# Performance work log

Measured on AMD Instinct MI355X. Metric: run time of the kernel, lower is better.

The kernel has to match this reference:

```python
import jax, jax.numpy as jnp
import numpy as np
from jax import lax

K, N, DV, NBPS, NITER, BATCH = 1056, 2112, 5, 4, 20, 1024
M = N - K            # number of parity checks
E = M * (DV + 1)     # Tanner-graph edges (H = [A | I_m], row weight DV+1)
NSYM = N // NBPS     # QAM symbols per codeword


def _qam16():
    # Sionna-style Gray-mapped QAM constellation, unit average energy.
    def pam_gray(b):
        if len(b) > 1:
            return (1 - 2 * b[0]) * (2 ** (len(b) - 1) - pam_gray(b[1:]))
        return 1 - 2 * b[0]
    pts = []
    for i in range(2 ** NBPS):
        b = [(i >> (NBPS - 1 - j)) & 1 for j in range(NBPS)]
        pts.append(complex(pam_gray(b[0::2]), pam_gray(b[1::2])))
    pts = np.asarray(pts)
    pts = pts / np.sqrt(np.mean(np.abs(pts) ** 2))
    return pts.real.astype(np.float32), pts.imag.astype(np.float32)


def setup_inputs() -> dict:
    key = jax.random.key(0)
    rng = np.random.default_rng(0)
    bits = jnp.asarray(rng.integers(0, 2, size=(BATCH, K)), jnp.int32)
    # sparse A: DV distinct info-bit columns per check row
    a_idx = np.argsort(rng.random((M, K)), axis=1)[:, :DV].astype(np.int32)
    edge_vn = np.concatenate([a_idx, K + np.arange(M, dtype=np.int32)[:, None]], axis=1).reshape(-1)
    edge_cn = np.repeat(np.arange(M, dtype=np.int32), DV + 1)
    pre, pim = _qam16()
    k1, k2 = jax.random.split(key)
    return {
        "bits": bits,
        "a_idx": jnp.asarray(a_idx),
        "edge_cn": jnp.asarray(edge_cn),
        "edge_vn": jnp.asarray(edge_vn),
        "points_re": jnp.asarray(pre),
        "points_im": jnp.asarray(pim),
        "noise_re": jax.random.normal(k1, (BATCH, NSYM), jnp.float32),
        "noise_im": jax.random.normal(k2, (BATCH, NSYM), jnp.float32),
        "ebno_db": jnp.float32(4.0),
    }


def _forward(bits, a_idx, edge_cn, edge_vn, points_re, points_im, noise_re, noise_im, ebno_db):
    B = bits.shape[0]
    coderate = K / N
    # ebnodb2no (Es = 1): N0 = 1 / (EbN0_lin * coderate * bits_per_symbol)
    no = 1.0 / (10.0 ** (ebno_db / 10.0) * coderate * NBPS)
    # --- LDPC encode: H = [A | I], parity_i = XOR of info bits in row i ---
    parity = jnp.sum(bits[:, a_idx], axis=-1) % 2          # [B, M]
    cw = jnp.concatenate([bits, parity], axis=1)           # [B, N]
    # --- QAM map ---
    w = jnp.array([1 << (NBPS - 1 - j) for j in range(NBPS)], jnp.int32)
    sym = jnp.sum(cw.reshape(B, NSYM, NBPS) * w, axis=-1)  # [B, S]
    sigma = jnp.sqrt(no / 2.0)
    y_re = points_re[sym] + sigma * noise_re
    y_im = points_im[sym] + sigma * noise_im
    # --- APP demap: LLR = log p(b=0|y) - log p(b=1|y) ---
    d2 = (y_re[..., None] - points_re) ** 2 + (y_im[..., None] - points_im) ** 2  # [B,S,16]
    lg = (-d2 / no)[..., None]                                                     # [B,S,16,1]
    lab = (jnp.arange(2 ** NBPS)[:, None] >> jnp.arange(NBPS - 1, -1, -1)) & 1     # [16,4]
    NEG = jnp.float32(-1e30)
    l0 = jax.nn.logsumexp(jnp.where(lab == 0, lg, NEG), axis=2)
    l1 = jax.nn.logsumexp(jnp.where(lab == 1, lg, NEG), axis=2)
    llr = (l0 - l1).reshape(B, N)                          # [B, N]
    # --- sum-product BP, flooding schedule, NITER iterations ---
    def marg(c2v):  # scatter-add check->variable messages onto variable nodes
        return jnp.zeros((B, N), c2v.dtype).at[:, edge_vn].add(c2v)
    def step(c2v, _):
        v2c = (llr + marg(c2v))[:, edge_vn] - c2v          # extrinsic VN->CN [B,E]
        av = jnp.clip(jnp.abs(v2c), 1e-6, 20.0)
        lt = jnp.log(jnp.tanh(av * 0.5))                   # log|tanh(.)| <= 0
        sg = (v2c < 0).astype(v2c.dtype)
        cs = jnp.zeros((B, M), v2c.dtype).at[:, edge_cn].add(lt)
        ns = jnp.zeros((B, M), v2c.dtype).at[:, edge_cn].add(sg)
        ex = jnp.exp(jnp.minimum(cs[:, edge_cn] - lt, -1e-7))   # prod over other edges < 1
        sp = 1.0 - 2.0 * jnp.mod(ns[:, edge_cn] - sg, 2.0)      # sign product over other edges
        return sp * 2.0 * jnp.arctanh(ex), None
    c2v, _ = lax.scan(step, jnp.zeros((B, E), jnp.float32), None, length=NITER)
    tot = llr + marg(c2v)
    bits_rx = (tot[:, :K] < 0).astype(jnp.float32)         # hard_out=True
    return bits.astype(jnp.float32), bits_rx, tot[:, :K]


def reference(bits, a_idx, edge_cn, edge_vn, points_re, points_im, noise_re, noise_im, ebno_db):
    b, brx, _ = _forward(bits, a_idx, edge_cn, edge_vn, points_re, points_im,
                         noise_re, noise_im, ebno_db)
    return b, brx
```

## Files before the change

kernel.cpp:

```cpp
#include <hip/hip_runtime.h>

#define K_     1056
#define N_     2112
#define M_     1056
#define E_     6336
#define NIE_   5280
#define CAP_   6336
#define ALL_   7392
#define DV_    5
#define ROW_   6
#define NSYM_  528
#define NITER_ 20
#define BATCH_ 1024
#define BS_    512

#define LOG2E_ 1.4426950408889634f
#define AVLO_  (1e-6f * LOG2E_)
#define AVHI_  (20.0f * LOG2E_)
#define QC_    0.99999988f

__device__ __forceinline__ int seg_stride(int d) { return d | 1; }

__device__ __forceinline__ float fexp2(float x) { return __builtin_amdgcn_exp2f(x); }
__device__ __forceinline__ float flog2(float x) { return __builtin_amdgcn_logf(x); }
__device__ __forceinline__ float frcp(float x)  { return __builtin_amdgcn_rcpf(x); }

__global__ __launch_bounds__(BS_, 8) void link_kernel(
    const int*   __restrict__ bits,
    const int*   __restrict__ a_idx,
    const float* __restrict__ points_re,
    const float* __restrict__ points_im,
    const float* __restrict__ noise_re,
    const float* __restrict__ noise_im,
    const float* __restrict__ ebno_db,
    const int*   __restrict__ edge_vn,
    float*       __restrict__ out)
{
#pragma clang fp contract(off)
    const int b   = blockIdx.x;
    const int tid = threadIdx.x;

    __shared__ float s_all[ALL_];
    __shared__ float s_pre[16];
    __shared__ float s_pim[16];
    __shared__ int   s_hist[32];
    __shared__ int   s_binStart[32];
    __shared__ int   s_binBase[32];

    float* s_mem  = s_all;
    float* s_marg = s_all + CAP_;

    int* sc        = (int*)(s_all + N_);
    int* s_deg     = sc;
    int* s_perm    = sc + K_;
    int* s_offslot = sc + 2 * K_;
    int* s_cnt     = sc + 3 * K_;

    if (tid < 16) {
        s_pre[tid] = points_re[tid];
        s_pim[tid] = points_im[tid];
    }
    if (tid < 32) s_hist[tid] = 0;

    const float eb    = ebno_db[0];
    const float no    = 1.0f / ((powf(10.0f, eb / 10.0f) * 0.5f) * 4.0f);
    const float sigma = sqrtf(no / 2.0f);

    for (int i = tid; i < K_; i += BS_) {
        int v = bits[b * K_ + i];
        s_mem[i] = (float)v;
        out[b * K_ + i] = (float)v;
    }
    __syncthreads();

    for (int m = tid; m < M_; m += BS_) {
        float acc = 0.0f;
        #pragma unroll
        for (int d = 0; d < DV_; ++d) acc += s_mem[a_idx[m * DV_ + d]];
        s_mem[K_ + m] = (float)(((int)acc) & 1);
    }
    for (int v = tid; v < K_; v += BS_) { s_deg[v] = 0; s_cnt[v] = 0; }
    __syncthreads();

    for (int s = tid; s < NSYM_; s += BS_) {
        int c0 = (int)s_mem[4 * s + 0];
        int c1 = (int)s_mem[4 * s + 1];
        int c2 = (int)s_mem[4 * s + 2];
        int c3 = (int)s_mem[4 * s + 3];
        int sym = c0 * 8 + c1 * 4 + c2 * 2 + c3;
        float yre = s_pre[sym] + sigma * noise_re[b * NSYM_ + s];
        float yim = s_pim[sym] + sigma * noise_im[b * NSYM_ + s];
        float m0[4], m1[4];
        #pragma unroll
        for (int j = 0; j < 4; ++j) { m0[j] = -1e30f; m1[j] = -1e30f; }
        #pragma unroll
        for (int p = 0; p < 16; ++p) {
            float dre  = yre - s_pre[p];
            float dim_ = yim - s_pim[p];
            float lg   = -(dre * dre + dim_ * dim_) / no;
            #pragma unroll
            for (int j = 0; j < 4; ++j) {
                if (((p >> (3 - j)) & 1) == 0) m0[j] = fmaxf(m0[j], lg);
                else                           m1[j] = fmaxf(m1[j], lg);
            }
        }
        float sum0[4] = {0.0f, 0.0f, 0.0f, 0.0f};
        float sum1[4] = {0.0f, 0.0f, 0.0f, 0.0f};
        #pragma unroll
        for (int p = 0; p < 16; ++p) {
            float dre  = yre - s_pre[p];
            float dim_ = yim - s_pim[p];
            float lg   = -(dre * dre + dim_ * dim_) / no;
            #pragma unroll
            for (int j = 0; j < 4; ++j) {
                if (((p >> (3 - j)) & 1) == 0) sum0[j] += __expf(lg - m0[j]);
                else                           sum1[j] += __expf(lg - m1[j]);
            }
        }
        #pragma unroll
        for (int j = 0; j < 4; ++j) {
            float llr = (m0[j] + __logf(sum0[j])) - (m1[j] + __logf(sum1[j]));
            s_mem[4 * s + j] = llr * LOG2E_;
        }
    }
    for (int idx = tid; idx < NIE_; idx += BS_) {
        int m = idx / 5, j = idx - m * 5;
        atomicAdd(&s_deg[edge_vn[m * ROW_ + j]], 1);
    }
    __syncthreads();

    for (int v = tid; v < K_; v += BS_) atomicAdd(&s_hist[s_deg[v] & 31], 1);
    __syncthreads();
    if (tid == 0) {
        int accS = 0, accB = 0;
        for (int d = 0; d < 32; ++d) {
            int c = s_hist[d];
            s_binStart[d] = accS;
            s_binBase[d]  = accB;
            s_hist[d]     = accS;
            accS += c;
            accB += c * seg_stride(d);
        }
    }
    __syncthreads();
    for (int v = tid; v < K_; v += BS_) {
        int d    = s_deg[v];
        int slot = atomicAdd(&s_hist[d & 31], 1);
        int base = s_binBase[d] + (slot - s_binStart[d]) * seg_stride(d);
        s_perm[slot]  = v | (d << 16);
        s_offslot[v]  = base | (slot << 16);
    }
    __syncthreads();

    int      pv[3];
    unsigned od[3];
    float    lr[3];
    #pragma unroll
    for (int k = 0; k < 3; ++k) {
        int s = tid + BS_ * k;
        if (s < K_) {
            int w = s_perm[s];
            int v = w & 0xFFFF;
            int d = w >> 16;
            int base = s_binBase[d] + (s - s_binStart[d]) * seg_stride(d);
            pv[k] = v;
            od[k] = (unsigned)base | ((unsigned)d << 16);
            lr[k] = s_mem[v];
        } else { pv[k] = 0; od[k] = 0; lr[k] = 0.0f; }
    }
    float    t5[3];
    unsigned vnp[3][5];
    #pragma unroll
    for (int kk = 0; kk < 3; ++kk) {
        int m = tid + BS_ * kk;
        if (m < M_) {
            #pragma unroll
            for (int j = 0; j < 5; ++j) {
                int v = edge_vn[m * ROW_ + j];
                int r = atomicAdd(&s_cnt[v], 1);
                int w = s_offslot[v];
                vnp[kk][j]  = (unsigned)(w >> 16) | ((unsigned)((w & 0xFFFF) + r) << 16);
            }
            float lrP = s_mem[K_ + m];
            float av  = __builtin_amdgcn_fmed3f(fabsf(lrP), AVLO_, AVHI_);
            float e   = fexp2(-av);
            float tm  = (1.0f - e) * frcp(1.0f + e);
            t5[kk] = copysignf(tm, lrP);
        } else { t5[kk] = 0.0f; }
    }
    __syncthreads();
    for (int i = tid; i < CAP_; i += BS_) s_mem[i] = 0.0f;
    __syncthreads();

    for (int it = 0; it < NITER_; ++it) {
        #pragma unroll
        for (int k = 0; k < 3; ++k) {
            int s = tid + BS_ * k;
            if (s < K_) {
                int base = (int)(od[k] & 0xFFFFu);
                int dg   = (int)(od[k] >> 16);
                float mg = lr[k];
                int d = 0;
                for (; d + 1 < dg; d += 2) {
                    mg += s_mem[base + d];
                    mg += s_mem[base + d + 1];
                }
                if (d < dg) mg += s_mem[base + d];
                s_marg[s] = mg;
            }
        }
        __syncthreads();
        #pragma unroll
        for (int kk = 0; kk < 3; ++kk) {
            int m = tid + BS_ * kk;
            if (m < M_) {
                float tj[5];
                #pragma unroll
                for (int j = 0; j < 5; ++j) {
                    unsigned w = vnp[kk][j];
                    float v2c = s_marg[w & 0xFFFFu] - s_mem[w >> 16];
                    float av  = __builtin_amdgcn_fmed3f(fabsf(v2c), AVLO_, AVHI_);
                    float e   = fexp2(-av);
                    float tm  = (1.0f - e) * frcp(1.0f + e);
                    tj[j] = copysignf(tm, v2c);
                }
                float qv[5];
                float pr = t5[kk];
                #pragma unroll
                for (int j = 0; j < 5; ++j) { qv[j] = pr; pr *= tj[j]; }
                float sf = 1.0f;
                #pragma unroll
                for (int j = 4; j >= 0; --j) { qv[j] *= sf; sf *= tj[j]; }
                #pragma unroll
                for (int j = 0; j < 5; ++j) {
                    float q = __builtin_amdgcn_fmed3f(qv[j], -QC_, QC_);
                    float r = flog2((1.0f + q) * frcp(1.0f - q));
                    s_mem[vnp[kk][j] >> 16] = r;
                }
            }
        }
        __syncthreads();
    }

    #pragma unroll
    for (int k = 0; k < 3; ++k) {
        int s = tid + BS_ * k;
        if (s < K_) {
            int base = (int)(od[k] & 0xFFFFu);
            int dg   = (int)(od[k] >> 16);
            float mg = lr[k];
            int d = 0;
            for (; d + 1 < dg; d += 2) {
                mg += s_mem[base + d];
                mg += s_mem[base + d + 1];
            }
            if (d < dg) mg += s_mem[base + d];
            out[(size_t)BATCH_ * K_ + b * K_ + pv[k]] = (mg < 0.0f) ? 1.0f : 0.0f;
        }
    }
}

extern "C" void kernel_launch(void* const* d_in, const int* in_sizes, int n_in,
                              void* d_out, int out_size, void* d_ws, size_t ws_size,
                              hipStream_t stream) {
    const int*   bits    = (const int*)  d_in[0];
    const int*   a_idx   = (const int*)  d_in[1];
    const int*   edge_vn = (const int*)  d_in[3];
    const float* pre     = (const float*)d_in[4];
    const float* pim     = (const float*)d_in[5];
    const float* nre     = (const float*)d_in[6];
    const float* nim     = (const float*)d_in[7];
    const float* ebno    = (const float*)d_in[8];

    link_kernel<<<BATCH_, BS_, 0, stream>>>(bits, a_idx, pre, pim, nre, nim,
                                            ebno, edge_vn, (float*)d_out);
}
```

Before: 185.5 us.

## Store check-to-variable messages in check-major order with ushort gather index

Messages are now stored contiguously per check node (edge m*5+j) rather than in variable-node-segmented slots. The VN marginal sum instead gathers through a shared ushort index table, while the CN update reads and writes its five messages contiguously and keeps only packed marginal slot indices in registers. This cuts per-thread register use (15 packed words down to 9) and makes CN-side shared accesses contiguous. In exchange the VN-side sum gains an extra indirect shared load per edge.

```diff
diff --git a/kernel.cpp b/kernel.cpp
--- a/kernel.cpp
+++ b/kernel.cpp
@@ -5,8 +5,7 @@
 #define M_     1056
 #define E_     6336
 #define NIE_   5280
-#define CAP_   6336
-#define ALL_   7392
+#define IDXCAP_ 6336
 #define DV_    5
 #define ROW_   6
 #define NSYM_  528
@@ -40,21 +39,20 @@
     const int b   = blockIdx.x;
     const int tid = threadIdx.x;
 
-    __shared__ float s_all[ALL_];
+    __shared__ float s_c2v[NIE_];
+    __shared__ float s_marg[K_];
+    __shared__ unsigned short s_idx[IDXCAP_];
     __shared__ float s_pre[16];
     __shared__ float s_pim[16];
     __shared__ int   s_hist[32];
     __shared__ int   s_binStart[32];
     __shared__ int   s_binBase[32];
 
-    float* s_mem  = s_all;
-    float* s_marg = s_all + CAP_;
-
-    int* sc        = (int*)(s_all + N_);
-    int* s_deg     = sc;
-    int* s_perm    = sc + K_;
-    int* s_offslot = sc + 2 * K_;
-    int* s_cnt     = sc + 3 * K_;
+    int* sc_tail   = (int*)s_c2v + N_;
+    int* s_deg     = sc_tail;
+    int* s_perm    = sc_tail + K_;
+    int* s_offslot = sc_tail + 2 * K_;
+    int* s_cnt     = (int*)s_marg;
 
     if (tid < 16) {
         s_pre[tid] = points_re[tid];
@@ -68,7 +66,7 @@
 
     for (int i = tid; i < K_; i += BS_) {
         int v = bits[b * K_ + i];
-        s_mem[i] = (float)v;
+        s_c2v[i] = (float)v;
         out[b * K_ + i] = (float)v;
     }
     __syncthreads();
@@ -76,17 +74,17 @@
     for (int m = tid; m < M_; m += BS_) {
         float acc = 0.0f;
         #pragma unroll
-        for (int d = 0; d < DV_; ++d) acc += s_mem[a_idx[m * DV_ + d]];
-        s_mem[K_ + m] = (float)(((int)acc) & 1);
+        for (int d = 0; d < DV_; ++d) acc += s_c2v[a_idx[m * DV_ + d]];
+        s_c2v[K_ + m] = (float)(((int)acc) & 1);
     }
     for (int v = tid; v < K_; v += BS_) { s_deg[v] = 0; s_cnt[v] = 0; }
     __syncthreads();
 
     for (int s = tid; s < NSYM_; s += BS_) {
-        int c0 = (int)s_mem[4 * s + 0];
-        int c1 = (int)s_mem[4 * s + 1];
-        int c2 = (int)s_mem[4 * s + 2];
-        int c3 = (int)s_mem[4 * s + 3];
+        int c0 = (int)s_c2v[4 * s + 0];
+        int c1 = (int)s_c2v[4 * s + 1];
+        int c2 = (int)s_c2v[4 * s + 2];
+        int c3 = (int)s_c2v[4 * s + 3];
         int sym = c0 * 8 + c1 * 4 + c2 * 2 + c3;
         float yre = s_pre[sym] + sigma * noise_re[b * NSYM_ + s];
         float yim = s_pim[sym] + sigma * noise_im[b * NSYM_ + s];
@@ -120,7 +118,7 @@
         #pragma unroll
         for (int j = 0; j < 4; ++j) {
             float llr = (m0[j] + __logf(sum0[j])) - (m1[j] + __logf(sum1[j]));
-            s_mem[4 * s + j] = llr * LOG2E_;
+            s_c2v[4 * s + j] = llr * LOG2E_;
         }
     }
     for (int idx = tid; idx < NIE_; idx += BS_) {
@@ -165,31 +163,38 @@
             int base = s_binBase[d] + (s - s_binStart[d]) * seg_stride(d);
             pv[k] = v;
             od[k] = (unsigned)base | ((unsigned)d << 16);
-            lr[k] = s_mem[v];
+            lr[k] = s_c2v[v];
         } else { pv[k] = 0; od[k] = 0; lr[k] = 0.0f; }
     }
     float    t5[3];
-    unsigned vnp[3][5];
+    unsigned sp0[3], sp1[3], sp2[3];
     #pragma unroll
     for (int kk = 0; kk < 3; ++kk) {
         int m = tid + BS_ * kk;
         if (m < M_) {
+            unsigned sl[5];
             #pragma unroll
-            for (int j = 0; j < 5; ++j) {
-                int v = edge_vn[m * ROW_ + j];
-                int r = atomicAdd(&s_cnt[v], 1);
-                int w = s_offslot[v];
-                vnp[kk][j]  = (unsigned)(w >> 16) | ((unsigned)((w & 0xFFFF) + r) << 16);
-            }
-            float lrP = s_mem[K_ + m];
+            for (int j = 0; j < 5; ++j)
+                sl[j] = (unsigned)(s_offslot[edge_vn[m * ROW_ + j]] >> 16);
+            sp0[kk] = sl[0] | (sl[1] << 16);
+            sp1[kk] = sl[2] | (sl[3] << 16);
+            sp2[kk] = sl[4];
+            float lrP = s_c2v[K_ + m];
             float av  = __builtin_amdgcn_fmed3f(fabsf(lrP), AVLO_, AVHI_);
             float e   = fexp2(-av);
             float tm  = (1.0f - e) * frcp(1.0f + e);
             t5[kk] = copysignf(tm, lrP);
-        } else { t5[kk] = 0.0f; }
-    }
-    __syncthreads();
-    for (int i = tid; i < CAP_; i += BS_) s_mem[i] = 0.0f;
+        } else { t5[kk] = 0.0f; sp0[kk] = sp1[kk] = sp2[kk] = 0u; }
+    }
+    for (int idx = tid; idx < NIE_; idx += BS_) {
+        int m = idx / 5, j = idx - m * 5;
+        int v = edge_vn[m * ROW_ + j];
+        int r = atomicAdd(&s_cnt[v], 1);
+        int w = s_offslot[v];
+        s_idx[(w & 0xFFFF) + r] = (unsigned short)(m * 5 + j);
+    }
+    __syncthreads();
+    for (int i = tid; i < NIE_; i += BS_) s_c2v[i] = 0.0f;
     __syncthreads();
 
     for (int it = 0; it < NITER_; ++it) {
@@ -202,10 +207,12 @@
                 float mg = lr[k];
                 int d = 0;
                 for (; d + 1 < dg; d += 2) {
-                    mg += s_mem[base + d];
-                    mg += s_mem[base + d + 1];
+                    int p0 = s_idx[base + d];
+                    int p1 = s_idx[base + d + 1];
+                    mg += s_c2v[p0];
+                    mg += s_c2v[p1];
                 }
-                if (d < dg) mg += s_mem[base + d];
+                if (d < dg) mg += s_c2v[s_idx[base + d]];
                 s_marg[s] = mg;
             }
         }
@@ -214,11 +221,17 @@
         for (int kk = 0; kk < 3; ++kk) {
             int m = tid + BS_ * kk;
             if (m < M_) {
+                int eb5 = m * 5;
+                int sl[5];
+                sl[0] = (int)(sp0[kk] & 0xFFFFu);
+                sl[1] = (int)(sp0[kk] >> 16);
+                sl[2] = (int)(sp1[kk] & 0xFFFFu);
+                sl[3] = (int)(sp1[kk] >> 16);
+                sl[4] = (int)sp2[kk];
                 float tj[5];
                 #pragma unroll
                 for (int j = 0; j < 5; ++j) {
-                    unsigned w = vnp[kk][j];
-                    float v2c = s_marg[w & 0xFFFFu] - s_mem[w >> 16];
+                    float v2c = s_marg[sl[j]] - s_c2v[eb5 + j];
                     float av  = __builtin_amdgcn_fmed3f(fabsf(v2c), AVLO_, AVHI_);
                     float e   = fexp2(-av);
                     float tm  = (1.0f - e) * frcp(1.0f + e);
@@ -235,7 +248,7 @@
                 for (int j = 0; j < 5; ++j) {
                     float q = __builtin_amdgcn_fmed3f(qv[j], -QC_, QC_);
                     float r = flog2((1.0f + q) * frcp(1.0f - q));
-                    s_mem[vnp[kk][j] >> 16] = r;
+                    s_c2v[eb5 + j] = r;
                 }
             }
         }
@@ -251,10 +264,12 @@
             float mg = lr[k];
             int d = 0;
             for (; d + 1 < dg; d += 2) {
-                mg += s_mem[base + d];
-                mg += s_mem[base + d + 1];
-            }
-            if (d < dg) mg += s_mem[base + d];
+                int p0 = s_idx[base + d];
+                int p1 = s_idx[base + d + 1];
+                mg += s_c2v[p0];
+                mg += s_c2v[p1];
+            }
+            if (d < dg) mg += s_c2v[s_idx[base + d]];
             out[(size_t)BATCH_ * K_ + b * K_ + pv[k]] = (mg < 0.0f) ? 1.0f : 0.0f;
         }
     }
```

New measurement: 198.1 us. +6.8%, slower.
